# Optimization experiments

Hardware: AMD Instinct MI355X
Metric: run time of the kernel (lower is better)

## Reference

```python
import jax, jax.numpy as jnp
import numpy as np
from jax import lax

NUM_CHARS = 128
BATCH = 1024
SEQ_LEN = 256
UNITS = 256


def setup_inputs() -> dict:
    key = jax.random.key(0)
    k1, k2, k3, k4 = jax.random.split(key, 4)
    inputs = jax.random.randint(k1, (BATCH, SEQ_LEN), 0, NUM_CHARS, dtype=jnp.int32)
    # LSTMCell params (Keras layout: gates ordered i, f, g(c), o along last dim)
    kernel = jax.random.normal(k2, (NUM_CHARS, 4 * UNITS), dtype=jnp.float32) * 0.05
    recurrent_kernel = jax.random.normal(k3, (UNITS, 4 * UNITS), dtype=jnp.float32) * 0.05
    bias = jnp.zeros((4 * UNITS,), dtype=jnp.float32)
    # unit_forget_bias=True in Keras default: forget-gate bias initialized to 1
    bias = bias.at[UNITS:2 * UNITS].set(1.0)
    dense_w = jax.random.normal(k4, (UNITS, NUM_CHARS), dtype=jnp.float32) * 0.05
    dense_b = jnp.zeros((NUM_CHARS,), dtype=jnp.float32)
    return {"inputs": inputs, "kernel": kernel, "recurrent_kernel": recurrent_kernel,
            "bias": bias, "dense_w": dense_w, "dense_b": dense_b}


def reference(inputs, kernel, recurrent_kernel, bias, dense_w, dense_b):
    # one_hot(inputs) @ kernel == row-gather of kernel; fuse with bias add.
    x_proj = kernel[inputs] + bias          # [B, T, 4U]
    B = inputs.shape[0]
    units = recurrent_kernel.shape[0]
    h0 = jnp.zeros((B, units), kernel.dtype)
    c0 = jnp.zeros((B, units), kernel.dtype)

    def step(carry, xp):
        h, c = carry
        z = xp + h @ recurrent_kernel        # [B, 4U]
        i, f, g, o = jnp.split(z, 4, axis=-1)
        i = jax.nn.sigmoid(i)
        f = jax.nn.sigmoid(f)
        g = jnp.tanh(g)
        o = jax.nn.sigmoid(o)
        c = f * c + i * g
        h = o * jnp.tanh(c)
        return (h, c), None

    (h_last, _), _ = lax.scan(step, (h0, c0), jnp.swapaxes(x_proj, 0, 1))
    logits = h_last @ dense_w + dense_b      # [B, num_chars]
    return jax.nn.softmax(logits)
```

## Files before the change

### kernel.cpp

```cpp
#include <hip/hip_runtime.h>
#include <math.h>

#define BATCH 1024
#define SEQ   256
#define UNITS 256
#define NC    128

typedef __attribute__((ext_vector_type(8))) short  short8;
typedef __attribute__((ext_vector_type(4))) float  float4v;
typedef unsigned long long u64;
typedef unsigned int       u32;

__device__ __forceinline__ float sigf(float x)  { return 1.f / (1.f + __expf(-x)); }
__device__ __forceinline__ float tanhf_(float x){ return 1.f - 2.f / (1.f + __expf(2.f * x)); }

__device__ __forceinline__ unsigned short bf16rne(float f) {
    unsigned u = __float_as_uint(f);
    return (unsigned short)((u + 0x7fffu + ((u >> 16) & 1u)) >> 16);
}
__device__ __forceinline__ float bf16tof(unsigned short s) {
    return __uint_as_float(((unsigned)s) << 16);
}

__global__ __launch_bounds__(256) void prep(
    const float* __restrict__ R, const float* __restrict__ Wk,
    const float* __restrict__ bias,
    unsigned short* __restrict__ R0t, unsigned short* __restrict__ R1t,
    float* __restrict__ Wkb, u32* __restrict__ H01A, u32* __restrict__ ctr)
{
    int i = blockIdx.x * 256 + threadIdx.x;
    int col = i >> 8, k = i & 255;
    float v = R[k * 1024 + col];
    unsigned short r0 = bf16rne(v);
    R0t[i] = r0;
    R1t[i] = bf16rne(v - bf16tof(r0));
    H01A[i] = 0u;
    if (i < NC * 1024) {
        int r = i & 1023;
        int u = r >> 2, g = r & 3;
        int src = (g << 8) + u;
        Wkb[i] = Wk[(i >> 10) * 1024 + src] + bias[src];
    }
    if (i < 1024) ctr[i] = 0u;
}

__global__ __launch_bounds__(256, 1) void lstm_persist(
    const unsigned short* __restrict__ R0t, const unsigned short* __restrict__ R1t,
    const float* __restrict__ Wkb, const int* __restrict__ inp,
    u32* __restrict__ H01A, u32* __restrict__ H01B, u32* __restrict__ ctr)
{
    __shared__ u32 Llo[16 * 132];
    __shared__ u32 Lhi[16 * 132];

    const int tid  = threadIdx.x;
    const int lane = tid & 63;
    const int wv   = tid >> 6;
    const int bI   = blockIdx.x;
    const int row  = ((bI & 7) << 3) | ((bI >> 3) & 7);
    const int ui   = bI >> 6;
    const int nl   = lane & 15;
    const int quad = lane >> 4;
    const int u    = ui * 64 + wv * 16 + nl;
    const int bm   = row * 16;
    const int be   = bm + (quad << 2);

    u32* const myctr = &ctr[row << 4];

    short8 B0[4][8], B1[4][8];
#pragma unroll
    for (int g = 0; g < 4; g++)
#pragma unroll
        for (int kt = 0; kt < 8; kt++) {
            const int idx = ((g << 8) + u) * 256 + (kt << 5) + (quad << 3);
            B0[g][kt] = *(const short8*)&R0t[idx];
            B1[g][kt] = *(const short8*)&R1t[idx];
        }
#pragma unroll
    for (int g = 0; g < 4; g++)
#pragma unroll
        for (int kt = 0; kt < 8; kt++) {
            asm volatile("" : "+a"(B0[g][kt]));
            asm volatile("" : "+a"(B1[g][kt]));
        }

    float c[4] = {0.f, 0.f, 0.f, 0.f};
    int ch[4];
#pragma unroll
    for (int r = 0; r < 4; r++) ch[r] = inp[(be + r) * SEQ];

    for (int t = 0; t < SEQ; t++) {
        const u32* Hin  = (t & 1) ? H01B : H01A;
        u32*       Hout = (t & 1) ? H01A : H01B;

        float4v wk[4];
#pragma unroll
        for (int r = 0; r < 4; r++)
            wk[r] = *(const float4v*)&Wkb[(ch[r] << 10) + (u << 2)];
        int chn[4];
        if (t != SEQ - 1) {
#pragma unroll
            for (int r = 0; r < 4; r++) chn[r] = inp[(be + r) * SEQ + t + 1];
        }

        if (t) {
            const u32 target = (u32)(t << 2);
            while (__hip_atomic_load(myctr, __ATOMIC_RELAXED,
                                     __HIP_MEMORY_SCOPE_AGENT) < target)
                __builtin_amdgcn_s_sleep(1);
        }

        {
            const u64* src = (const u64*)(Hin + (bm << 8));
#pragma unroll
            for (int i = 0; i < 8; i++) {
                const int e = tid + (i << 8);
                u64 q = __hip_atomic_load(src + e, __ATOMIC_RELAXED,
                                          __HIP_MEMORY_SCOPE_AGENT);
                u32 w0 = (u32)q, w1 = (u32)(q >> 32);
                const int rr = e >> 7, cp = e & 127;
                Llo[rr * 132 + cp] = (w0 & 0xffffu) | (w1 << 16);
                Lhi[rr * 132 + cp] = (w0 >> 16) | (w1 & 0xffff0000u);
            }
        }
        __syncthreads();

        float4v acc[4];
#pragma unroll
        for (int kt = 0; kt < 8; kt++) {
            short8 a0 = *(const short8*)&Llo[nl * 132 + (kt << 4) + (quad << 2)];
            short8 a1 = *(const short8*)&Lhi[nl * 132 + (kt << 4) + (quad << 2)];
            if (kt == 0) {
#pragma unroll
                for (int g = 0; g < 4; g++) {
                    asm volatile("v_mfma_f32_16x16x32_bf16 %0, %1, %2, 0"
                                 : "=v"(acc[g]) : "v"(a0), "a"(B0[g][0]));
                    asm volatile("v_mfma_f32_16x16x32_bf16 %0, %1, %2, %0"
                                 : "+v"(acc[g]) : "v"(a1), "a"(B0[g][0]));
                    asm volatile("v_mfma_f32_16x16x32_bf16 %0, %1, %2, %0"
                                 : "+v"(acc[g]) : "v"(a0), "a"(B1[g][0]));
                }
            } else {
#pragma unroll
                for (int g = 0; g < 4; g++) {
                    asm volatile("v_mfma_f32_16x16x32_bf16 %0, %1, %2, %0"
                                 : "+v"(acc[g]) : "v"(a0), "a"(B0[g][kt]));
                    asm volatile("v_mfma_f32_16x16x32_bf16 %0, %1, %2, %0"
                                 : "+v"(acc[g]) : "v"(a1), "a"(B0[g][kt]));
                    asm volatile("v_mfma_f32_16x16x32_bf16 %0, %1, %2, %0"
                                 : "+v"(acc[g]) : "v"(a0), "a"(B1[g][kt]));
                }
            }
        }
        asm volatile("s_nop 7\n\ts_nop 7\n\ts_nop 3" ::: );

#pragma unroll
        for (int r = 0; r < 4; r++) {
            float zi = acc[0][r] + wk[r].x;
            float zf = acc[1][r] + wk[r].y;
            float zg = acc[2][r] + wk[r].z;
            float zo = acc[3][r] + wk[r].w;
            float ig = sigf(zi), fg = sigf(zf), gg = tanhf_(zg), og = sigf(zo);
            float cn = fg * c[r] + ig * gg;
            c[r] = cn;
            float hv = og * tanhf_(cn);
            unsigned short h0 = bf16rne(hv);
            unsigned short h1 = bf16rne(hv - bf16tof(h0));
            u32 packed = (u32)h0 | ((u32)h1 << 16);
            __hip_atomic_store(&Hout[(be + r) * 256 + u], packed,
                               __ATOMIC_RELAXED, __HIP_MEMORY_SCOPE_AGENT);
        }

        if (t != SEQ - 1) {
            __syncthreads();
            if (tid == 0)
                __hip_atomic_fetch_add(myctr, 1u, __ATOMIC_RELAXED,
                                       __HIP_MEMORY_SCOPE_AGENT);
#pragma unroll
            for (int r = 0; r < 4; r++) ch[r] = chn[r];
        }
    }
}

__global__ __launch_bounds__(128) void dense_softmax(
    const u32* __restrict__ H01, const float* __restrict__ W,
    const float* __restrict__ b, float* __restrict__ out)
{
    __shared__ float hsr[UNITS];
    __shared__ float red[NC];
    const int bq = blockIdx.x;
    const int n  = threadIdx.x;

    u32 v0 = H01[bq * 256 + n];
    u32 v1 = H01[bq * 256 + n + 128];
    hsr[n]       = bf16tof((unsigned short)(v0 & 0xffffu)) + bf16tof((unsigned short)(v0 >> 16));
    hsr[n + 128] = bf16tof((unsigned short)(v1 & 0xffffu)) + bf16tof((unsigned short)(v1 >> 16));
    __syncthreads();

    float acc = b[n];
#pragma unroll 8
    for (int k = 0; k < UNITS; k++) acc += hsr[k] * W[k * NC + n];

    red[n] = acc;
    __syncthreads();
    for (int s = 64; s > 0; s >>= 1) {
        if (n < s) red[n] = fmaxf(red[n], red[n + s]);
        __syncthreads();
    }
    float m = red[0];
    __syncthreads();

    float e = __expf(acc - m);
    red[n] = e;
    __syncthreads();
    for (int s = 64; s > 0; s >>= 1) {
        if (n < s) red[n] = red[n] + red[n + s];
        __syncthreads();
    }
    out[bq * NC + n] = e / red[0];
}

extern "C" void kernel_launch(void* const* d_in, const int* in_sizes, int n_in,
                              void* d_out, int out_size, void* d_ws, size_t ws_size,
                              hipStream_t stream)
{
    const int*   inp  = (const int*)d_in[0];
    const float* Wk   = (const float*)d_in[1];
    const float* R    = (const float*)d_in[2];
    const float* bias = (const float*)d_in[3];
    const float* Wd   = (const float*)d_in[4];
    const float* bd   = (const float*)d_in[5];
    float* out = (float*)d_out;

    unsigned short* R0t  = (unsigned short*)d_ws;
    unsigned short* R1t  = R0t + 262144;
    float*          Wkb  = (float*)(R1t + 262144);
    u32*            H01A = (u32*)(Wkb + 131072);
    u32*            H01B = H01A + 262144;
    u32*            ctr  = H01B + 262144;

    prep<<<dim3(1024), dim3(256), 0, stream>>>(R, Wk, bias, R0t, R1t, Wkb, H01A, ctr);

    lstm_persist<<<dim3(256), dim3(256), 0, stream>>>(R0t, R1t, Wkb, inp,
                                                      H01A, H01B, ctr);

    dense_softmax<<<dim3(BATCH), dim3(128), 0, stream>>>(H01A, Wd, bd, out);
}
```

Measured before the change: 1.181 ms.

## Interleave two batch row-groups per block to overlap h exchange with compute

```diff
diff --git a/kernel.cpp b/kernel.cpp
--- a/kernel.cpp
+++ b/kernel.cpp
@@ -49,22 +49,18 @@
     const float* __restrict__ Wkb, const int* __restrict__ inp,
     u32* __restrict__ H01A, u32* __restrict__ H01B, u32* __restrict__ ctr)
 {
-    __shared__ u32 Llo[16 * 132];
-    __shared__ u32 Lhi[16 * 132];
+    __shared__ u32 L[2][2][16 * 132];
 
     const int tid  = threadIdx.x;
     const int lane = tid & 63;
     const int wv   = tid >> 6;
     const int bI   = blockIdx.x;
-    const int row  = ((bI & 7) << 3) | ((bI >> 3) & 7);
-    const int ui   = bI >> 6;
+    const int pr   = bI & 31;
+    const int ui   = bI >> 5;
     const int nl   = lane & 15;
     const int quad = lane >> 4;
     const int u    = ui * 64 + wv * 16 + nl;
-    const int bm   = row * 16;
-    const int be   = bm + (quad << 2);
-
-    u32* const myctr = &ctr[row << 4];
+    const int row0 = pr << 1, row1 = row0 | 1;
 
     short8 B0[4][8], B1[4][8];
 #pragma unroll
@@ -83,52 +79,66 @@
             asm volatile("" : "+a"(B1[g][kt]));
         }
 
-    float c[4] = {0.f, 0.f, 0.f, 0.f};
-    int ch[4];
-#pragma unroll
-    for (int r = 0; r < 4; r++) ch[r] = inp[(be + r) * SEQ];
-
-    for (int t = 0; t < SEQ; t++) {
-        const u32* Hin  = (t & 1) ? H01B : H01A;
-        u32*       Hout = (t & 1) ? H01A : H01B;
+    float c[2][4] = {{0.f,0.f,0.f,0.f},{0.f,0.f,0.f,0.f}};
+
+    u64 q[8];
+    {
+        const u64* src = (const u64*)(H01A + (row0 << 12));
+#pragma unroll
+        for (int i = 0; i < 8; i++)
+            q[i] = __hip_atomic_load(src + tid + (i << 8), __ATOMIC_RELAXED,
+                                     __HIP_MEMORY_SCOPE_AGENT);
+    }
+
+    for (int ph = 0; ph < 2 * SEQ; ph++) {
+        const int t    = ph >> 1;
+        const int cur  = ph & 1;
+        const int rowC = cur ? row1 : row0;
+        const int be   = (rowC << 4) + (quad << 2);
+
+        int ch[4];
+#pragma unroll
+        for (int r = 0; r < 4; r++) ch[r] = inp[(be + r) * SEQ + t];
+
+#pragma unroll
+        for (int i = 0; i < 8; i++) {
+            const int e = tid + (i << 8);
+            u32 w0 = (u32)q[i], w1 = (u32)(q[i] >> 32);
+            const int rr = e >> 7, cp = e & 127;
+            L[cur][0][rr * 132 + cp] = (w0 & 0xffffu) | (w1 << 16);
+            L[cur][1][rr * 132 + cp] = (w0 >> 16) | (w1 & 0xffff0000u);
+        }
+        __syncthreads();
+
+        {
+            const int rowO = cur ? row0 : row1;
+            const int tO   = cur ? t + 1 : t;
+            if (tO < SEQ) {
+                if (tO > 0) {
+                    u32* poc = &ctr[rowO << 4];
+                    const u32 target = (u32)(tO << 2);
+                    while (__hip_atomic_load(poc, __ATOMIC_RELAXED,
+                                             __HIP_MEMORY_SCOPE_AGENT) < target)
+                        __builtin_amdgcn_s_sleep(1);
+                }
+                const u64* src = (const u64*)(((tO & 1) ? H01B : H01A) + (rowO << 12));
+#pragma unroll
+                for (int i = 0; i < 8; i++)
+                    q[i] = __hip_atomic_load(src + tid + (i << 8), __ATOMIC_RELAXED,
+                                             __HIP_MEMORY_SCOPE_AGENT);
+            }
+        }
 
         float4v wk[4];
 #pragma unroll
         for (int r = 0; r < 4; r++)
             wk[r] = *(const float4v*)&Wkb[(ch[r] << 10) + (u << 2)];
-        int chn[4];
-        if (t != SEQ - 1) {
-#pragma unroll
-            for (int r = 0; r < 4; r++) chn[r] = inp[(be + r) * SEQ + t + 1];
-        }
-
-        if (t) {
-            const u32 target = (u32)(t << 2);
-            while (__hip_atomic_load(myctr, __ATOMIC_RELAXED,
-                                     __HIP_MEMORY_SCOPE_AGENT) < target)
-                __builtin_amdgcn_s_sleep(1);
-        }
-
-        {
-            const u64* src = (const u64*)(Hin + (bm << 8));
-#pragma unroll
-            for (int i = 0; i < 8; i++) {
-                const int e = tid + (i << 8);
-                u64 q = __hip_atomic_load(src + e, __ATOMIC_RELAXED,
-                                          __HIP_MEMORY_SCOPE_AGENT);
-                u32 w0 = (u32)q, w1 = (u32)(q >> 32);
-                const int rr = e >> 7, cp = e & 127;
-                Llo[rr * 132 + cp] = (w0 & 0xffffu) | (w1 << 16);
-                Lhi[rr * 132 + cp] = (w0 >> 16) | (w1 & 0xffff0000u);
-            }
-        }
-        __syncthreads();
 
         float4v acc[4];
 #pragma unroll
         for (int kt = 0; kt < 8; kt++) {
-            short8 a0 = *(const short8*)&Llo[nl * 132 + (kt << 4) + (quad << 2)];
-            short8 a1 = *(const short8*)&Lhi[nl * 132 + (kt << 4) + (quad << 2)];
+            short8 a0 = *(const short8*)&L[cur][0][nl * 132 + (kt << 4) + (quad << 2)];
+            short8 a1 = *(const short8*)&L[cur][1][nl * 132 + (kt << 4) + (quad << 2)];
             if (kt == 0) {
 #pragma unroll
                 for (int g = 0; g < 4; g++) {
@@ -138,6 +148,8 @@
                                  : "+v"(acc[g]) : "v"(a1), "a"(B0[g][0]));
                     asm volatile("v_mfma_f32_16x16x32_bf16 %0, %1, %2, %0"
                                  : "+v"(acc[g]) : "v"(a0), "a"(B1[g][0]));
+                    asm volatile("v_mfma_f32_16x16x32_bf16 %0, %1, %2, %0"
+                                 : "+v"(acc[g]) : "v"(a1), "a"(B1[g][0]));
                 }
             } else {
 #pragma unroll
@@ -148,11 +160,15 @@
                                  : "+v"(acc[g]) : "v"(a1), "a"(B0[g][kt]));
                     asm volatile("v_mfma_f32_16x16x32_bf16 %0, %1, %2, %0"
                                  : "+v"(acc[g]) : "v"(a0), "a"(B1[g][kt]));
+                    asm volatile("v_mfma_f32_16x16x32_bf16 %0, %1, %2, %0"
+                                 : "+v"(acc[g]) : "v"(a1), "a"(B1[g][kt]));
                 }
             }
         }
-        asm volatile("s_nop 7\n\ts_nop 7\n\ts_nop 3" ::: );
-
+        asm volatile("s_nop 7\n\ts_nop 7\n\ts_nop 7"
+                     : "+v"(acc[0]), "+v"(acc[1]), "+v"(acc[2]), "+v"(acc[3]));
+
+        u32* Hout = (t & 1) ? H01A : H01B;
 #pragma unroll
         for (int r = 0; r < 4; r++) {
             float zi = acc[0][r] + wk[r].x;
@@ -160,8 +176,8 @@
             float zg = acc[2][r] + wk[r].z;
             float zo = acc[3][r] + wk[r].w;
             float ig = sigf(zi), fg = sigf(zf), gg = tanhf_(zg), og = sigf(zo);
-            float cn = fg * c[r] + ig * gg;
-            c[r] = cn;
+            float cn = fg * c[cur][r] + ig * gg;
+            c[cur][r] = cn;
             float hv = og * tanhf_(cn);
             unsigned short h0 = bf16rne(hv);
             unsigned short h1 = bf16rne(hv - bf16tof(h0));
@@ -173,10 +189,8 @@
         if (t != SEQ - 1) {
             __syncthreads();
             if (tid == 0)
-                __hip_atomic_fetch_add(myctr, 1u, __ATOMIC_RELAXED,
+                __hip_atomic_fetch_add(&ctr[rowC << 4], 1u, __ATOMIC_RELAXED,
                                        __HIP_MEMORY_SCOPE_AGENT);
-#pragma unroll
-            for (int r = 0; r < 4; r++) ch[r] = chn[r];
         }
     }
 }
@@ -240,7 +254,7 @@
 
     prep<<<dim3(1024), dim3(256), 0, stream>>>(R, Wk, bias, R0t, R1t, Wkb, H01A, ctr);
 
-    lstm_persist<<<dim3(256), dim3(256), 0, stream>>>(R0t, R1t, Wkb, inp,
+    lstm_persist<<<dim3(128), dim3(256), 0, stream>>>(R0t, R1t, Wkb, inp,
                                                       H01A, H01B, ctr);
 
     dense_softmax<<<dim3(BATCH), dim3(128), 0, stream>>>(H01A, Wd, bd, out);
```

Measured after the change: 1.741 ms. +47.4%, slower.
